# Performance work log

Measured on AMD Instinct MI355X. Metric: run time of the kernel, lower is better.

Reference implementation:

```python
import jax, jax.numpy as jnp
import numpy as np
from jax import lax

B, S, DIMS, T, K = 4, 4096, 2048, 10, 2


def setup_inputs() -> dict:
    key = jax.random.key(0)
    ks = jax.random.split(key, 4)
    scale = 1.0 / np.sqrt(DIMS)
    x = jax.random.normal(ks[0], (B, S, DIMS), dtype=jnp.float32)
    W_cls = jax.random.normal(ks[1], (DIMS, T), dtype=jnp.float32) * scale
    W_sparse = jax.random.normal(ks[2], (DIMS, T), dtype=jnp.float32) * scale
    W_gates = jax.random.normal(ks[3], (DIMS, T), dtype=jnp.float32) * scale
    return {
        "x": x,
        "W_cls": W_cls, "b_cls": jnp.zeros((T,), jnp.float32),
        "W_sparse": W_sparse, "b_sparse": jnp.zeros((T,), jnp.float32),
        "W_gates": W_gates, "b_gates": jnp.zeros((T,), jnp.float32),
        "alpha": jnp.ones((1,), jnp.float32),
    }


def reference(x, W_cls, b_cls, W_sparse, b_sparse, W_gates, b_gates, alpha):
    # soft routing: softmax classifier over num_types
    soft_types = jax.nn.softmax(jnp.einsum("bsd,dt->bst", x, W_cls) + b_cls, axis=-1)
    # sparse routing: top-k over logits, softmax over the k kept logits,
    # scattered back into a dense [B,S,T] gate vector (zeros elsewhere)
    logits = jnp.einsum("bsd,dt->bst", x, W_sparse) + b_sparse
    top_v, top_i = lax.top_k(logits, K)                      # [B,S,K]
    sparse_g = jax.nn.softmax(top_v, axis=-1)                # [B,S,K]
    # scatter via one-hot (K and T are tiny)
    sparse_types = jnp.sum(jax.nn.one_hot(top_i, T, dtype=x.dtype) * sparse_g[..., None], axis=-2)  # [B,S,T]
    # per-type sigmoid gates: batched single matmul == stack of Linear(dims,1)+Sigmoid
    gates = jax.nn.sigmoid(jnp.einsum("bsd,dt->bst", x, W_gates) + b_gates)  # [B,S,T]
    a = jax.nn.sigmoid(alpha)                                # [1], broadcasts
    mixed_types = a * sparse_types + (1.0 - a) * soft_types  # [B,S,T]
    # original: gates stacked as [B,S,1,T], mixed unsqueezed to [B,S,1,T], sum over T -> [B,S,1]
    return jnp.sum(gates * mixed_types, axis=-1, keepdims=True)
```

## Files before the change

kernel.cpp:

```cpp
#include <hip/hip_runtime.h>
#include <math.h>
#include <stdint.h>


#define NROWS   16384
#define DIMS_   2048
#define TT      10
#define NCOL    32
#define KSL     8
#define KPS     8
#define PITCH   132

typedef __attribute__((ext_vector_type(8))) short short8;
typedef __attribute__((ext_vector_type(4))) float f32x4;

__device__ __forceinline__ unsigned short bf16_rne(float f) {
    unsigned int u = __float_as_uint(f);
    unsigned int r = u + 0x7fffu + ((u >> 16) & 1u);
    return (unsigned short)(r >> 16);
}

__global__ __launch_bounds__(256)
void tgate_k0(const float* __restrict__ W_cls,
              const float* __restrict__ W_sparse,
              const float* __restrict__ W_gates,
              unsigned short* __restrict__ frag)
{
    int t = blockIdx.x * 256 + threadIdx.x;
    int K0   = t >> 7;
    int nt   = (t >> 6) & 1;
    int lane = t & 63;
    int n  = nt * 16 + (lane & 15);
    int kb = K0 * 32 + (lane >> 4) * 8;
    short8 hi, lo;
    #pragma unroll
    for (int j = 0; j < 8; ++j) {
        int k = kb + j;
        float w = 0.0f;
        if (n < 10)      w = W_cls[k * TT + n];
        else if (n < 20) w = W_sparse[k * TT + n - 10];
        else if (n < 30) w = W_gates[k * TT + n - 20];
        unsigned short h = bf16_rne(w);
        float back = __uint_as_float(((unsigned int)h) << 16);
        hi[j] = (short)h;
        lo[j] = (short)bf16_rne(w - back);
    }
    short8* fv = reinterpret_cast<short8*>(frag);
    fv[(K0 * 4 + nt * 2 + 0) * 64 + lane] = hi;
    fv[(K0 * 4 + nt * 2 + 1) * 64 + lane] = lo;
}

__global__ __launch_bounds__(256)
void tgate_k1(const float* __restrict__ x,
              const unsigned short* __restrict__ frag,
              float* __restrict__ part)
{
    __shared__ float lds[4][16 * PITCH];

    const int lane  = threadIdx.x & 63;
    const int wv    = __builtin_amdgcn_readfirstlane(threadIdx.x >> 6);
    const int bx    = blockIdx.x;
    const int row0  = (bx * 4 + wv) * 16;
    const int slice = (blockIdx.y + bx) & 7;
    const int m     = lane & 15;
    const int quad  = lane >> 4;

    float* L = lds[wv];

    const int rs = lane >> 5;
    const int cs = (lane & 31) * 4;

    const float4* x4 = reinterpret_cast<const float4*>(x);
    const int cb0 = slice * 256;

    float4 pre[8];
    #pragma unroll
    for (int t = 0; t < 8; ++t)
        pre[t] = x4[(size_t)(row0 + 2 * t + rs) * 512 + ((cb0 + cs) >> 2)];

    const short8* fv = reinterpret_cast<const short8*>(frag);
    f32x4 acc0 = {0.f, 0.f, 0.f, 0.f};
    f32x4 acc1 = {0.f, 0.f, 0.f, 0.f};

    #pragma unroll
    for (int ch = 0; ch < 2; ++ch) {
        #pragma unroll
        for (int t = 0; t < 8; ++t)
            *reinterpret_cast<float4*>(&L[(2 * t + rs) * PITCH + cs]) = pre[t];
        if (ch == 0) {
            #pragma unroll
            for (int t = 0; t < 8; ++t)
                pre[t] = x4[(size_t)(row0 + 2 * t + rs) * 512 + ((cb0 + 128 + cs) >> 2)];
        }
        #pragma unroll
        for (int ksl = 0; ksl < 4; ++ksl) {
            const int K0 = slice * KPS + ch * 4 + ksl;
            const float* src = &L[m * PITCH + ksl * 32 + quad * 8];
            float4 b0 = *reinterpret_cast<const float4*>(src);
            float4 b1 = *reinterpret_cast<const float4*>(src + 4);
            float f[8] = {b0.x, b0.y, b0.z, b0.w, b1.x, b1.y, b1.z, b1.w};
            short8 ah, al;
            #pragma unroll
            for (int j = 0; j < 8; ++j) {
                unsigned short h = bf16_rne(f[j]);
                float back = __uint_as_float(((unsigned int)h) << 16);
                ah[j] = (short)h;
                al[j] = (short)bf16_rne(f[j] - back);
            }
            short8 fh0 = fv[(K0 * 4 + 0) * 64 + lane];
            short8 fl0 = fv[(K0 * 4 + 1) * 64 + lane];
            short8 fh1 = fv[(K0 * 4 + 2) * 64 + lane];
            short8 fl1 = fv[(K0 * 4 + 3) * 64 + lane];
            acc0 = __builtin_amdgcn_mfma_f32_16x16x32_bf16(ah, fh0, acc0, 0, 0, 0);
            acc0 = __builtin_amdgcn_mfma_f32_16x16x32_bf16(al, fh0, acc0, 0, 0, 0);
            acc0 = __builtin_amdgcn_mfma_f32_16x16x32_bf16(ah, fl0, acc0, 0, 0, 0);
            acc1 = __builtin_amdgcn_mfma_f32_16x16x32_bf16(ah, fh1, acc1, 0, 0, 0);
            acc1 = __builtin_amdgcn_mfma_f32_16x16x32_bf16(al, fh1, acc1, 0, 0, 0);
            acc1 = __builtin_amdgcn_mfma_f32_16x16x32_bf16(ah, fl1, acc1, 0, 0, 0);
        }
    }

    #pragma unroll
    for (int r = 0; r < 4; ++r) {
        int row = row0 + quad * 4 + r;
        float* p = part + ((size_t)slice * NROWS + row) * NCOL;
        p[m]      = acc0[r];
        p[m + 16] = acc1[r];
    }
}

__global__ __launch_bounds__(256)
void tgate_k2(const float* __restrict__ part,
              const float* __restrict__ b_cls,
              const float* __restrict__ b_sparse,
              const float* __restrict__ b_gates,
              const float* __restrict__ alpha,
              float* __restrict__ out)
{
    const int r = blockIdx.x * 256 + threadIdx.x;
    const float4* p4 = reinterpret_cast<const float4*>(part);

    float l[32];
    #pragma unroll
    for (int j = 0; j < 32; ++j) l[j] = 0.0f;
    #pragma unroll
    for (int s = 0; s < KSL; ++s) {
        size_t base = ((size_t)s * NROWS + r) * 8;
        #pragma unroll
        for (int q = 0; q < 8; ++q) {
            float4 v = p4[base + q];
            l[q * 4 + 0] += v.x; l[q * 4 + 1] += v.y;
            l[q * 4 + 2] += v.z; l[q * 4 + 3] += v.w;
        }
    }

    float lc[TT], lsp[TT], g[TT];
    #pragma unroll
    for (int t = 0; t < TT; ++t) {
        lc[t]  = l[t]      + b_cls[t];
        lsp[t] = l[10 + t] + b_sparse[t];
        float lg = l[20 + t] + b_gates[t];
        g[t] = 1.0f / (1.0f + __expf(-lg));
    }
    float m = lc[0];
    #pragma unroll
    for (int t = 1; t < TT; ++t) m = fmaxf(m, lc[t]);
    float esum = 0.0f, gdot = 0.0f;
    #pragma unroll
    for (int t = 0; t < TT; ++t) {
        float e = __expf(lc[t] - m);
        esum += e;
        gdot = fmaf(g[t], e, gdot);
    }
    float v1 = lsp[0], v2 = -1e30f, gv1 = g[0], gv2 = 0.0f;
    #pragma unroll
    for (int t = 1; t < TT; ++t) {
        if (lsp[t] > v1)      { v2 = v1; gv2 = gv1; v1 = lsp[t]; gv1 = g[t]; }
        else if (lsp[t] > v2) { v2 = lsp[t]; gv2 = g[t]; }
    }
    float s1 = 1.0f / (1.0f + __expf(v2 - v1));
    float s2 = 1.0f - s1;
    float a  = 1.0f / (1.0f + __expf(-alpha[0]));
    float sparse_dot = fmaf(gv1, s1, gv2 * s2);
    out[r] = fmaf(a, sparse_dot, (1.0f - a) * (gdot / esum));
}

extern "C" void kernel_launch(void* const* d_in, const int* in_sizes, int n_in,
                              void* d_out, int out_size, void* d_ws, size_t ws_size,
                              hipStream_t stream) {
    const float* x        = (const float*)d_in[0];
    const float* W_cls    = (const float*)d_in[1];
    const float* b_cls    = (const float*)d_in[2];
    const float* W_sparse = (const float*)d_in[3];
    const float* b_sparse = (const float*)d_in[4];
    const float* W_gates  = (const float*)d_in[5];
    const float* b_gates  = (const float*)d_in[6];
    const float* alpha    = (const float*)d_in[7];
    float* out = (float*)d_out;

    unsigned short* frag = (unsigned short*)d_ws;
    float* part = (float*)((char*)d_ws + (512 << 10));

    tgate_k0<<<dim3(32), dim3(256), 0, stream>>>(W_cls, W_sparse, W_gates, frag);
    tgate_k1<<<dim3(NROWS / 64, KSL), dim3(256), 0, stream>>>(x, frag, part);
    tgate_k2<<<dim3(NROWS / 256), dim3(256), 0, stream>>>(part, b_cls, b_sparse,
                                                          b_gates, alpha, out);
}
```

Before: 219.4 us.

## Fuse split-K reduction and routing epilogue into the MFMA kernel via LDS

Each block now covers 16 rows across the full 2048-wide reduction. Its four waves each take a 512-column range and software-prefetch four 128-column chunks. Per-wave accumulators are reduced in shared memory, and the softmax/top-2/sigmoid epilogue runs in the same kernel. This removes the global partial-sum buffer (write plus read) and the third kernel launch. In exchange the grid has half as many blocks and each wave does more serial work, so fewer memory requests are in flight. It also adds block-level barriers and leaves only 16 threads active for the epilogue.

```diff
diff --git a/kernel.cpp b/kernel.cpp
--- a/kernel.cpp
+++ b/kernel.cpp
@@ -6,9 +6,6 @@
 #define NROWS   16384
 #define DIMS_   2048
 #define TT      10
-#define NCOL    32
-#define KSL     8
-#define KPS     8
 #define PITCH   132
 
 typedef __attribute__((ext_vector_type(8))) short short8;
@@ -53,48 +50,56 @@
 __global__ __launch_bounds__(256)
 void tgate_k1(const float* __restrict__ x,
               const unsigned short* __restrict__ frag,
-              float* __restrict__ part)
+              const float* __restrict__ b_cls,
+              const float* __restrict__ b_sparse,
+              const float* __restrict__ b_gates,
+              const float* __restrict__ alpha,
+              float* __restrict__ out)
 {
     __shared__ float lds[4][16 * PITCH];
 
-    const int lane  = threadIdx.x & 63;
-    const int wv    = __builtin_amdgcn_readfirstlane(threadIdx.x >> 6);
-    const int bx    = blockIdx.x;
-    const int row0  = (bx * 4 + wv) * 16;
-    const int slice = (blockIdx.y + bx) & 7;
+    const int tid   = threadIdx.x;
+    const int lane  = tid & 63;
+    const int wv    = __builtin_amdgcn_readfirstlane(tid >> 6);
+    const int row0  = blockIdx.x * 16;
     const int m     = lane & 15;
     const int quad  = lane >> 4;
 
     float* L = lds[wv];
-
     const int rs = lane >> 5;
     const int cs = (lane & 31) * 4;
-
     const float4* x4 = reinterpret_cast<const float4*>(x);
-    const int cb0 = slice * 256;
+    const int cb = wv * 512;
 
     float4 pre[8];
     #pragma unroll
     for (int t = 0; t < 8; ++t)
-        pre[t] = x4[(size_t)(row0 + 2 * t + rs) * 512 + ((cb0 + cs) >> 2)];
+        pre[t] = x4[(size_t)(row0 + 2 * t + rs) * 512 + ((cb + cs) >> 2)];
 
     const short8* fv = reinterpret_cast<const short8*>(frag);
-    f32x4 acc0 = {0.f, 0.f, 0.f, 0.f};
-    f32x4 acc1 = {0.f, 0.f, 0.f, 0.f};
-
-    #pragma unroll
-    for (int ch = 0; ch < 2; ++ch) {
+    f32x4 acc[2][2];
+    #pragma unroll
+    for (int h = 0; h < 2; ++h) {
+        acc[h][0] = (f32x4){0.f, 0.f, 0.f, 0.f};
+        acc[h][1] = (f32x4){0.f, 0.f, 0.f, 0.f};
+    }
+
+    #pragma unroll
+    for (int c = 0; c < 4; ++c) {
         #pragma unroll
         for (int t = 0; t < 8; ++t)
             *reinterpret_cast<float4*>(&L[(2 * t + rs) * PITCH + cs]) = pre[t];
-        if (ch == 0) {
+        if (c < 3) {
             #pragma unroll
             for (int t = 0; t < 8; ++t)
-                pre[t] = x4[(size_t)(row0 + 2 * t + rs) * 512 + ((cb0 + 128 + cs) >> 2)];
-        }
+                pre[t] = x4[(size_t)(row0 + 2 * t + rs) * 512
+                            + ((cb + (c + 1) * 128 + cs) >> 2)];
+        }
+        const int h = c >> 1;
+        const int s = 2 * wv + h;
         #pragma unroll
         for (int ksl = 0; ksl < 4; ++ksl) {
-            const int K0 = slice * KPS + ch * 4 + ksl;
+            const int K0 = s * 8 + (c & 1) * 4 + ksl;
             const float* src = &L[m * PITCH + ksl * 32 + quad * 8];
             float4 b0 = *reinterpret_cast<const float4*>(src);
             float4 b1 = *reinterpret_cast<const float4*>(src + 4);
@@ -102,87 +107,82 @@
             short8 ah, al;
             #pragma unroll
             for (int j = 0; j < 8; ++j) {
-                unsigned short h = bf16_rne(f[j]);
-                float back = __uint_as_float(((unsigned int)h) << 16);
-                ah[j] = (short)h;
+                unsigned short hh = bf16_rne(f[j]);
+                float back = __uint_as_float(((unsigned int)hh) << 16);
+                ah[j] = (short)hh;
                 al[j] = (short)bf16_rne(f[j] - back);
             }
             short8 fh0 = fv[(K0 * 4 + 0) * 64 + lane];
             short8 fl0 = fv[(K0 * 4 + 1) * 64 + lane];
             short8 fh1 = fv[(K0 * 4 + 2) * 64 + lane];
             short8 fl1 = fv[(K0 * 4 + 3) * 64 + lane];
-            acc0 = __builtin_amdgcn_mfma_f32_16x16x32_bf16(ah, fh0, acc0, 0, 0, 0);
-            acc0 = __builtin_amdgcn_mfma_f32_16x16x32_bf16(al, fh0, acc0, 0, 0, 0);
-            acc0 = __builtin_amdgcn_mfma_f32_16x16x32_bf16(ah, fl0, acc0, 0, 0, 0);
-            acc1 = __builtin_amdgcn_mfma_f32_16x16x32_bf16(ah, fh1, acc1, 0, 0, 0);
-            acc1 = __builtin_amdgcn_mfma_f32_16x16x32_bf16(al, fh1, acc1, 0, 0, 0);
-            acc1 = __builtin_amdgcn_mfma_f32_16x16x32_bf16(ah, fl1, acc1, 0, 0, 0);
-        }
-    }
-
-    #pragma unroll
-    for (int r = 0; r < 4; ++r) {
-        int row = row0 + quad * 4 + r;
-        float* p = part + ((size_t)slice * NROWS + row) * NCOL;
-        p[m]      = acc0[r];
-        p[m + 16] = acc1[r];
-    }
-}
-
-__global__ __launch_bounds__(256)
-void tgate_k2(const float* __restrict__ part,
-              const float* __restrict__ b_cls,
-              const float* __restrict__ b_sparse,
-              const float* __restrict__ b_gates,
-              const float* __restrict__ alpha,
-              float* __restrict__ out)
-{
-    const int r = blockIdx.x * 256 + threadIdx.x;
-    const float4* p4 = reinterpret_cast<const float4*>(part);
-
-    float l[32];
-    #pragma unroll
-    for (int j = 0; j < 32; ++j) l[j] = 0.0f;
-    #pragma unroll
-    for (int s = 0; s < KSL; ++s) {
-        size_t base = ((size_t)s * NROWS + r) * 8;
-        #pragma unroll
-        for (int q = 0; q < 8; ++q) {
-            float4 v = p4[base + q];
-            l[q * 4 + 0] += v.x; l[q * 4 + 1] += v.y;
-            l[q * 4 + 2] += v.z; l[q * 4 + 3] += v.w;
-        }
-    }
-
-    float lc[TT], lsp[TT], g[TT];
-    #pragma unroll
-    for (int t = 0; t < TT; ++t) {
-        lc[t]  = l[t]      + b_cls[t];
-        lsp[t] = l[10 + t] + b_sparse[t];
-        float lg = l[20 + t] + b_gates[t];
-        g[t] = 1.0f / (1.0f + __expf(-lg));
-    }
-    float m = lc[0];
-    #pragma unroll
-    for (int t = 1; t < TT; ++t) m = fmaxf(m, lc[t]);
-    float esum = 0.0f, gdot = 0.0f;
-    #pragma unroll
-    for (int t = 0; t < TT; ++t) {
-        float e = __expf(lc[t] - m);
-        esum += e;
-        gdot = fmaf(g[t], e, gdot);
-    }
-    float v1 = lsp[0], v2 = -1e30f, gv1 = g[0], gv2 = 0.0f;
-    #pragma unroll
-    for (int t = 1; t < TT; ++t) {
-        if (lsp[t] > v1)      { v2 = v1; gv2 = gv1; v1 = lsp[t]; gv1 = g[t]; }
-        else if (lsp[t] > v2) { v2 = lsp[t]; gv2 = g[t]; }
-    }
-    float s1 = 1.0f / (1.0f + __expf(v2 - v1));
-    float s2 = 1.0f - s1;
-    float a  = 1.0f / (1.0f + __expf(-alpha[0]));
-    float sparse_dot = fmaf(gv1, s1, gv2 * s2);
-    out[r] = fmaf(a, sparse_dot, (1.0f - a) * (gdot / esum));
+            acc[h][0] = __builtin_amdgcn_mfma_f32_16x16x32_bf16(ah, fh0, acc[h][0], 0, 0, 0);
+            acc[h][0] = __builtin_amdgcn_mfma_f32_16x16x32_bf16(al, fh0, acc[h][0], 0, 0, 0);
+            acc[h][0] = __builtin_amdgcn_mfma_f32_16x16x32_bf16(ah, fl0, acc[h][0], 0, 0, 0);
+            acc[h][1] = __builtin_amdgcn_mfma_f32_16x16x32_bf16(ah, fh1, acc[h][1], 0, 0, 0);
+            acc[h][1] = __builtin_amdgcn_mfma_f32_16x16x32_bf16(al, fh1, acc[h][1], 0, 0, 0);
+            acc[h][1] = __builtin_amdgcn_mfma_f32_16x16x32_bf16(ah, fl1, acc[h][1], 0, 0, 0);
+        }
+    }
+
+    float* red = &lds[0][0];
+    __syncthreads();
+    #pragma unroll
+    for (int h = 0; h < 2; ++h) {
+        int s = 2 * wv + h;
+        #pragma unroll
+        for (int r = 0; r < 4; ++r) {
+            int row = quad * 4 + r;
+            red[(s * 16 + row) * 33 + m]      = acc[h][0][r];
+            red[(s * 16 + row) * 33 + m + 16] = acc[h][1][r];
+        }
+    }
+    __syncthreads();
+
+    float* fold = red + 8 * 16 * 33;
+    #pragma unroll
+    for (int u = 0; u < 2; ++u) {
+        int i = tid * 2 + u;
+        int row = i >> 5, j = i & 31;
+        float a = 0.0f;
+        #pragma unroll
+        for (int s = 0; s < 8; ++s) a += red[(s * 16 + row) * 33 + j];
+        fold[row * 33 + j] = a;
+    }
+    __syncthreads();
+
+    if (tid < 16) {
+        const float* l = &fold[tid * 33];
+        float lc[TT], lsp[TT], g[TT];
+        #pragma unroll
+        for (int t = 0; t < TT; ++t) {
+            lc[t]  = l[t]      + b_cls[t];
+            lsp[t] = l[10 + t] + b_sparse[t];
+            float lg = l[20 + t] + b_gates[t];
+            g[t] = 1.0f / (1.0f + __expf(-lg));
+        }
+        float mm = lc[0];
+        #pragma unroll
+        for (int t = 1; t < TT; ++t) mm = fmaxf(mm, lc[t]);
+        float esum = 0.0f, gdot = 0.0f;
+        #pragma unroll
+        for (int t = 0; t < TT; ++t) {
+            float e = __expf(lc[t] - mm);
+            esum += e;
+            gdot = fmaf(g[t], e, gdot);
+        }
+        float v1 = lsp[0], v2 = -1e30f, gv1 = g[0], gv2 = 0.0f;
+        #pragma unroll
+        for (int t = 1; t < TT; ++t) {
+            if (lsp[t] > v1)      { v2 = v1; gv2 = gv1; v1 = lsp[t]; gv1 = g[t]; }
+            else if (lsp[t] > v2) { v2 = lsp[t]; gv2 = g[t]; }
+        }
+        float s1 = 1.0f / (1.0f + __expf(v2 - v1));
+        float s2 = 1.0f - s1;
+        float a  = 1.0f / (1.0f + __expf(-alpha[0]));
+        float sparse_dot = fmaf(gv1, s1, gv2 * s2);
+        out[row0 + tid] = fmaf(a, sparse_dot, (1.0f - a) * (gdot / esum));
+    }
 }
 
 extern "C" void kernel_launch(void* const* d_in, const int* in_sizes, int n_in,
@@ -199,10 +199,8 @@
     float* out = (float*)d_out;
 
     unsigned short* frag = (unsigned short*)d_ws;
-    float* part = (float*)((char*)d_ws + (512 << 10));
 
     tgate_k0<<<dim3(32), dim3(256), 0, stream>>>(W_cls, W_sparse, W_gates, frag);
-    tgate_k1<<<dim3(NROWS / 64, KSL), dim3(256), 0, stream>>>(x, frag, part);
-    tgate_k2<<<dim3(NROWS / 256), dim3(256), 0, stream>>>(part, b_cls, b_sparse,
-                                                          b_gates, alpha, out);
-}
+    tgate_k1<<<dim3(NROWS / 16), dim3(256), 0, stream>>>(x, frag, b_cls, b_sparse,
+                                                         b_gates, alpha, out);
+}
```

Result: faster. 209.0 us (-4.8%).
